# Kernel optimization log

Measured on AMD Instinct MI355X. Metric: run time of the kernel, lower is better.

Reference implementation:

```python
import jax, jax.numpy as jnp
import numpy as np

R, K, CF, HF, WF = 64, 81, 256, 256, 256  # ROIs, classes(incl bg), FPN channels, P2 size
IMG = 1024.0
SCALE = 0.25          # P2 feature stride 4
STEPS = 4             # subdivision steps: 7 -> 112
NPTS = 28 * 28        # subdivision_num_points
FC = 256


def _grid_sample(img, coords):
    """torch.grid_sample(bilinear, align_corners=False, zeros padding).
    img: [N,C,H,W]; coords: [N,P,2] (x,y) in [0,1]. Returns [N,C,P]."""
    N, C, H, W = img.shape
    x = coords[..., 0] * W - 0.5
    y = coords[..., 1] * H - 0.5
    x0 = jnp.floor(x); y0 = jnp.floor(y)
    fx = x - x0; fy = y - y0

    def g(ix, iy, w):
        valid = (ix >= 0) & (ix < W) & (iy >= 0) & (iy < H)
        ixc = jnp.clip(ix, 0, W - 1).astype(jnp.int32)
        iyc = jnp.clip(iy, 0, H - 1).astype(jnp.int32)
        v = jax.vmap(lambda im, yy, xx: im[:, yy, xx])(img, iyc, ixc)  # [N,C,P]
        return v * (w * valid)[:, None, :]

    return (g(x0, y0, (1 - fx) * (1 - fy)) + g(x0 + 1, y0, fx * (1 - fy))
            + g(x0, y0 + 1, (1 - fx) * fy) + g(x0 + 1, y0 + 1, fx * fy))


def _point_head(fine, coarse, W1, b1, W2, b2, W3, b3, Wp, bp):
    # StandardPointHead: 1x1-conv fc layers, coarse logits re-concatenated each layer
    x = jnp.concatenate([fine, coarse], axis=1)  # [R, CF+K, P]
    for Wl, bl in ((W1, b1), (W2, b2), (W3, b3)):
        x = jax.nn.relu(jnp.einsum('oc,rcp->rop', Wl, x) + bl[None, :, None])
        x = jnp.concatenate([x, coarse], axis=1)
    return jnp.einsum('oc,rcp->rop', Wp, x) + bp[None, :, None]  # [R,K,P]


def setup_inputs() -> dict:
    key = jax.random.key(0)
    ks = jax.random.split(key, 12)
    feat = jax.random.normal(ks[0], (1, CF, HF, WF), dtype=jnp.float32)
    u = jax.random.uniform(ks[1], (R, 4), dtype=jnp.float32)
    x0 = u[:, 0] * (IMG - 256.0); y0 = u[:, 1] * (IMG - 256.0)
    w = 32.0 + u[:, 2] * 224.0;   h = 32.0 + u[:, 3] * 224.0
    det_bboxes = jnp.stack([x0, y0, x0 + w, y0 + h], axis=1)
    det_labels = jax.random.randint(ks[2], (R,), 0, 80, dtype=jnp.int32)
    coarse_logits = jax.random.normal(ks[3], (R, K, 7, 7), dtype=jnp.float32)
    cin = CF + K  # = FC + K = 337 for all layers here
    s = 0.02
    return {
        'feat': feat, 'det_bboxes': det_bboxes, 'det_labels': det_labels,
        'coarse_logits': coarse_logits,
        'W1': jax.random.normal(ks[4], (FC, cin), jnp.float32) * s,
        'b1': jnp.zeros((FC,), jnp.float32),
        'W2': jax.random.normal(ks[5], (FC, FC + K), jnp.float32) * s,
        'b2': jnp.zeros((FC,), jnp.float32),
        'W3': jax.random.normal(ks[6], (FC, FC + K), jnp.float32) * s,
        'b3': jnp.zeros((FC,), jnp.float32),
        'Wp': jax.random.normal(ks[7], (K, FC + K), jnp.float32) * s,
        'bp': jnp.zeros((K,), jnp.float32),
    }


def reference(feat, det_bboxes, det_labels, coarse_logits,
              W1, b1, W2, b2, W3, b3, Wp, bp):
    ml = coarse_logits
    bx0, by0 = det_bboxes[:, 0], det_bboxes[:, 1]
    bw = det_bboxes[:, 2] - det_bboxes[:, 0]
    bh = det_bboxes[:, 3] - det_bboxes[:, 1]
    for step in range(STEPS):
        _, _, H, W = ml.shape
        H, W = 2 * H, 2 * W
        # bilinear x2, align_corners=False (half-pixel centers)
        ml = jax.image.resize(ml, (R, K, H, W), method='linear')
        if NPTS >= 4 * H * W and step < STEPS - 1:
            continue
        # uncertainty = -|logit of gt class| (det_labels+1 skips background ch 0)
        gt = ml[jnp.arange(R), det_labels + 1]              # [R,H,W]
        unc = -jnp.abs(gt).reshape(R, H * W)
        _, idx = jax.lax.top_k(unc, NPTS)                   # [R,NPTS]
        px = ((idx % W).astype(ml.dtype) + 0.5) / W
        py = ((idx // W).astype(ml.dtype) + 0.5) / H
        coords = jnp.stack([px, py], axis=-1)               # [R,NPTS,2] in ROI [0,1]
        # project ROI coords to image, then to P2 normalized coords
        cx = bx0[:, None] + coords[..., 0] * bw[:, None]
        cy = by0[:, None] + coords[..., 1] * bh[:, None]
        fcoords = jnp.stack([cx * SCALE / WF, cy * SCALE / HF], axis=-1)
        fine = _grid_sample(feat, fcoords.reshape(1, R * NPTS, 2))  # [1,CF,R*NPTS]
        fine = fine[0].reshape(CF, R, NPTS).transpose(1, 0, 2)      # [R,CF,NPTS]
        coarse = _grid_sample(coarse_logits, coords)                # [R,K,NPTS]
        pl = _point_head(fine, coarse, W1, b1, W2, b2, W3, b3, Wp, bp)
        ml = jax.vmap(lambda m, i, p: m.at[:, i].set(p))(
            ml.reshape(R, K, H * W), idx, pl).reshape(R, K, H, W)
    return ml
```

## Files before the change

kernel.cpp:

```cpp
#include <hip/hip_runtime.h>
#include <hip/hip_bf16.h>
#include <cstdint>
#include <cstddef>

#define R_ 64
#define K_ 81
#define NPTS_ 784

typedef __attribute__((ext_vector_type(8))) short short8;
typedef __attribute__((ext_vector_type(4))) float f32x4;

#define GLDS16(G, L)                                                           \
  __builtin_amdgcn_global_load_lds(                                            \
      (__attribute__((address_space(1))) void*)(void*)(G),                     \
      (__attribute__((address_space(3))) void*)(L), 16, 0, 0)

__global__ __launch_bounds__(256) void transpose_feat_kernel(const float* __restrict__ in,
                                                             float* __restrict__ out) {
  __shared__ float tile[32][33];
  int y = blockIdx.z;
  int x0 = blockIdx.x * 32, c0 = blockIdx.y * 32;
  int tx = threadIdx.x, ty = threadIdx.y;
#pragma unroll
  for (int j = 0; j < 32; j += 8)
    tile[ty + j][tx] = in[(size_t)(c0 + ty + j) * 65536 + (size_t)y * 256 + x0 + tx];
  __syncthreads();
#pragma unroll
  for (int j = 0; j < 32; j += 8)
    out[((size_t)y * 256 + (x0 + ty + j)) * 256 + c0 + tx] = tile[tx][ty + j];
}

__global__ void prep_all_kernel(const float* __restrict__ W1, const float* __restrict__ W2,
                                const float* __restrict__ W3, const float* __restrict__ Wp,
                                const float* __restrict__ b1, const float* __restrict__ b2,
                                const float* __restrict__ b3, const float* __restrict__ bp,
                                const float* __restrict__ coarse_in,
                                __hip_bfloat16* __restrict__ Wpk, float* __restrict__ bias_all,
                                float* __restrict__ coarseT) {
  int t = blockIdx.x * 256 + threadIdx.x;
  if (t < 90112) {
    int lane = t & 63;
    int t2 = t >> 6;
    int hl = t2 & 1;
    t2 >>= 1;
    int jg = t2 & 15;
    t2 >>= 4;
    int kt = t2 % 11;
    int L = t2 / 11;
    int o = jg * 16 + (lane & 15);
    int kbase = kt * 32 + (lane >> 4) * 8;
    const float* Wsrc = (L == 0) ? W1 : (L == 1) ? W2 : (L == 2) ? W3 : Wp;
    int Omax = (L == 3) ? 81 : 256;
    __hip_bfloat16 outv[8];
#pragma unroll
    for (int e = 0; e < 8; ++e) {
      int k = kbase + e;
      float v = (o < Omax && k < 337) ? Wsrc[o * 337 + k] : 0.f;
      __hip_bfloat16 h = __float2bfloat16(v);
      outv[e] = hl ? __float2bfloat16(v - __bfloat162float(h)) : h;
    }
    *(short8*)(Wpk + (size_t)t * 8) = *(const short8*)outv;
  } else if (t < 90112 + 1024) {
    int k = t - 90112;
    float v = 0.f;
    if (k < 256) v = b1[k];
    else if (k < 512) v = b2[k - 256];
    else if (k < 768) v = b3[k - 512];
    else if (k < 768 + 81) v = bp[k - 768];
    bias_all[k] = v;
  } else {
    int t2 = t - 91136;
    if (t2 < R_ * 49 * K_) {
      int k = t2 % K_;
      int t3 = t2 / K_;
      int pos = t3 % 49;
      int r = t3 / 49;
      coarseT[t2] = coarse_in[((size_t)r * K_ + k) * 49 + pos];
    }
  }
}

__device__ __forceinline__ void quad_upsample(const float* __restrict__ p, int Hin, int Win,
                                              int iy, int ix, float& oTE, float& oTO,
                                              float& oBE, float& oBO) {
  int rT = (iy == 0) ? 0 : iy - 1;
  int rB = (iy == Hin - 1) ? iy : iy + 1;
  int cL = (ix == 0) ? 0 : ix - 1;
  int cR = (ix == Win - 1) ? ix : ix + 1;
  float wyT1 = (iy == 0) ? 0.f : 0.75f;
  float wyB1 = (iy == Hin - 1) ? 0.f : 0.25f;
  float wxE1 = (ix == 0) ? 0.f : 0.75f;
  float wxO1 = (ix == Win - 1) ? 0.f : 0.25f;
  float wyT0 = 1.f - wyT1, wyB0 = 1.f - wyB1;
  float wxE0 = 1.f - wxE1, wxO0 = 1.f - wxO1;
  const float* rowA = p + (size_t)rT * Win;
  const float* rowM = p + (size_t)iy * Win;
  const float* rowC = p + (size_t)rB * Win;
  float al = rowA[cL], am = rowA[ix], ar = rowA[cR];
  float mL = rowM[cL], mm = rowM[ix], mr = rowM[cR];
  float cl = rowC[cL], cm = rowC[ix], cr = rowC[cR];
  float aE = wxE0 * al + wxE1 * am;
  float aO = wxO0 * am + wxO1 * ar;
  float mE = wxE0 * mL + wxE1 * mm;
  float mO = wxO0 * mm + wxO1 * mr;
  float cE = wxE0 * cl + wxE1 * cm;
  float cO = wxO0 * cm + wxO1 * cr;
  oTE = wyT0 * aE + wyT1 * mE;
  oTO = wyT0 * aO + wyT1 * mO;
  oBE = wyB0 * mE + wyB1 * cE;
  oBO = wyB0 * mO + wyB1 * cO;
}

__global__ __launch_bounds__(128) void upsample2x_kernel(const float* __restrict__ in,
                                                         float* __restrict__ out,
                                                         int Hin, int Win) {
  int b = blockIdx.z;
  int iy = blockIdx.y * 2 + threadIdx.y;
  int ix = blockIdx.x * 64 + threadIdx.x;
  if (ix >= Win || iy >= Hin) return;
  const float* p = in + (size_t)b * Hin * Win;
  float oTE, oTO, oBE, oBO;
  quad_upsample(p, Hin, Win, iy, ix, oTE, oTO, oBE, oBO);
  int Wout = 2 * Win;
  float* ob = out + ((size_t)b * (2 * Hin) + 2 * iy) * Wout + 2 * ix;
  *(float2*)ob = make_float2(oTE, oTO);
  *(float2*)(ob + Wout) = make_float2(oBE, oBO);
}

__global__ __launch_bounds__(128) void upsample2x_gt_kernel(const float* __restrict__ ml56,
                                                            const int* __restrict__ labels,
                                                            float* __restrict__ gtbuf) {
  int r = blockIdx.z;
  int iy = blockIdx.y * 2 + threadIdx.y;
  int ix = blockIdx.x * 64 + threadIdx.x;
  if (ix >= 56 || iy >= 56) return;
  const float* p = ml56 + ((size_t)r * K_ + (labels[r] + 1)) * 3136;
  float oTE, oTO, oBE, oBO;
  quad_upsample(p, 56, 56, iy, ix, oTE, oTO, oBE, oBO);
  float* ob = gtbuf + ((size_t)r * 112 + 2 * iy) * 112 + 2 * ix;
  *(float2*)ob = make_float2(oTE, oTO);
  *(float2*)(ob + 112) = make_float2(oBE, oBO);
}

__global__ __launch_bounds__(128) void upsample2x_sel_kernel(const float* __restrict__ ml56,
                                                             const unsigned short* __restrict__ map,
                                                             const float* __restrict__ PL,
                                                             float* __restrict__ out) {
  int b = blockIdx.z;
  int r = b / K_;
  int k = b - r * K_;
  int iy = blockIdx.y * 2 + threadIdx.y;
  int ix = blockIdx.x * 64 + threadIdx.x;
  if (ix >= 56 || iy >= 56) return;
  const float* p = ml56 + (size_t)b * 3136;
  float oTE, oTO, oBE, oBO;
  quad_upsample(p, 56, 56, iy, ix, oTE, oTO, oBE, oBO);
  int oy = 2 * iy, ox = 2 * ix;
  const unsigned short* mr = map + (size_t)r * 12544;
  unsigned short r0 = mr[oy * 112 + ox], r1 = mr[oy * 112 + ox + 1];
  unsigned short r2 = mr[(oy + 1) * 112 + ox], r3 = mr[(oy + 1) * 112 + ox + 1];
  if (r0 != 0xFFFFu) oTE = PL[((size_t)r * NPTS_ + r0) * 128 + k];
  if (r1 != 0xFFFFu) oTO = PL[((size_t)r * NPTS_ + r1) * 128 + k];
  if (r2 != 0xFFFFu) oBE = PL[((size_t)r * NPTS_ + r2) * 128 + k];
  if (r3 != 0xFFFFu) oBO = PL[((size_t)r * NPTS_ + r3) * 128 + k];
  float* ob = out + ((size_t)b * 112 + oy) * 112 + ox;
  *(float2*)ob = make_float2(oTE, oTO);
  *(float2*)(ob + 112) = make_float2(oBE, oBO);
}

__global__ void mapinit_kernel(unsigned short* __restrict__ map) {
  int t = blockIdx.x * 256 + threadIdx.x;
  if (t < R_ * 12544) map[t] = 0xFFFFu;
}
__global__ void mapbuild_kernel(const int* __restrict__ sel, unsigned short* __restrict__ map) {
  int t = blockIdx.x * 256 + threadIdx.x;
  if (t < R_ * NPTS_) {
    int r = t / NPTS_;
    map[(size_t)r * 12544 + sel[t]] = (unsigned short)(t % NPTS_);
  }
}

__global__ __launch_bounds__(1024) void topk_kernel(const float* __restrict__ ml,
                                                    const int* __restrict__ labels,
                                                    const float* __restrict__ gtdirect,
                                                    int N, int* __restrict__ sel) {
  int r = blockIdx.x;
  const float* gt = gtdirect ? (gtdirect + (size_t)r * N)
                             : (ml + ((size_t)r * K_ + (labels[r] + 1)) * N);
  __shared__ unsigned int hist[256];
  __shared__ unsigned int sh_prefix, sh_remaining, sh_countless;
  __shared__ unsigned int wtot_less[16], wtot_eq[16];
  const int tid = threadIdx.x;
  const int lane = tid & 63;
  const int wv = tid >> 6;

  unsigned int prefix = 0;
  unsigned int remaining = NPTS_;
  unsigned int count_less = 0;
  for (int pass = 0; pass < 4; ++pass) {
    int shift = 24 - 8 * pass;
    if (tid < 256) hist[tid] = 0;
    __syncthreads();
    for (int i = tid; i < N; i += 1024) {
      unsigned int v = __float_as_uint(fabsf(gt[i]));
      bool match = (pass == 0) || ((v >> (shift + 8)) == prefix);
      unsigned int dg = (v >> shift) & 255u;
      if (pass == 0) {
        bool active = match;
        while (true) {
          unsigned long long act = __ballot(active);
          if (!act) break;
          int leader = (int)(__ffsll((long long)act) - 1);
          unsigned int ld = __shfl(dg, leader);
          bool same = active && (dg == ld);
          unsigned long long sm = __ballot(same);
          if (lane == leader) atomicAdd(&hist[ld], (unsigned int)__popcll(sm));
          active = active && !same;
        }
      } else if (match) {
        atomicAdd(&hist[dg], 1u);
      }
    }
    __syncthreads();
    if (tid < 64) {
      unsigned int s0 = hist[4 * lane + 0], s1 = hist[4 * lane + 1];
      unsigned int s2 = hist[4 * lane + 2], s3 = hist[4 * lane + 3];
      unsigned int ls = s0 + s1 + s2 + s3;
      unsigned int inc = ls;
#pragma unroll
      for (int d = 1; d < 64; d <<= 1) {
        unsigned int tv = __shfl_up(inc, d);
        if (lane >= d) inc += tv;
      }
      unsigned int exc = inc - ls;
      bool cross = (exc < remaining) && (exc + ls >= remaining);
      if (cross) {
        unsigned int before = exc;
        int d = 4 * lane;
        if (before + s0 < remaining) {
          before += s0; d++;
          if (before + s1 < remaining) {
            before += s1; d++;
            if (before + s2 < remaining) { before += s2; d++; }
          }
        }
        sh_prefix = (prefix << 8) | (unsigned int)d;
        sh_remaining = remaining - before;
        sh_countless = count_less + before;
      }
    }
    __syncthreads();
    prefix = sh_prefix;
    remaining = sh_remaining;
    count_less = sh_countless;
    __syncthreads();
  }
  unsigned int vstar = prefix;
  unsigned int need_eq = NPTS_ - count_less;

  unsigned int base_less = 0, base_eq = 0;
  int* selr = sel + (size_t)r * NPTS_;
  for (int base = 0; base < N; base += 1024) {
    int i = base + tid;
    bool less = false, eq = false;
    if (i < N) {
      unsigned int v = __float_as_uint(fabsf(gt[i]));
      less = v < vstar;
      eq = v == vstar;
    }
    unsigned long long ml_ = __ballot(less);
    unsigned long long me_ = __ballot(eq);
    unsigned long long lanemask = (lane == 0) ? 0ull : ((~0ull) >> (64 - lane));
    unsigned int pl = __popcll(ml_ & lanemask);
    unsigned int pe = __popcll(me_ & lanemask);
    if (lane == 0) {
      wtot_less[wv] = (unsigned int)__popcll(ml_);
      wtot_eq[wv] = (unsigned int)__popcll(me_);
    }
    __syncthreads();
    unsigned int off_l = 0, off_e = 0, tot_l = 0, tot_e = 0;
#pragma unroll
    for (int w2 = 0; w2 < 16; ++w2) {
      unsigned int tl = wtot_less[w2], te = wtot_eq[w2];
      if (w2 < wv) { off_l += tl; off_e += te; }
      tot_l += tl;
      tot_e += te;
    }
    if (less) selr[base_less + off_l + pl] = i;
    if (eq) {
      unsigned int er = base_eq + off_e + pe;
      if (er < need_eq) selr[count_less + er] = i;
    }
    base_less += tot_l;
    base_eq += tot_e;
    __syncthreads();
  }
}

__global__ __launch_bounds__(256) void sample_kernel(const int* __restrict__ sel,
                                                     const float* __restrict__ bboxes,
                                                     const float* __restrict__ featT,
                                                     const float* __restrict__ coarseT,
                                                     __hip_bfloat16* __restrict__ Xh,
                                                     __hip_bfloat16* __restrict__ Xl,
                                                     __hip_bfloat16* __restrict__ Cth,
                                                     __hip_bfloat16* __restrict__ Ctl,
                                                     int Wlev, int Hlev) {
  int rp = blockIdx.x;
  int r = rp / NPTS_;
  int idx = sel ? sel[rp] : (rp % NPTS_);
  int tid = threadIdx.x;

  float px = ((float)(idx % Wlev) + 0.5f) / (float)Wlev;
  float py = ((float)(idx / Wlev) + 0.5f) / (float)Hlev;
  float bx0 = bboxes[r * 4 + 0], by0 = bboxes[r * 4 + 1];
  float bw = __fsub_rn(bboxes[r * 4 + 2], bx0);
  float bh = __fsub_rn(bboxes[r * 4 + 3], by0);
  float cx = __fadd_rn(bx0, __fmul_rn(px, bw));
  float cy = __fadd_rn(by0, __fmul_rn(py, bh));

  {
    float gx = __fsub_rn(__fmul_rn(cx, 0.25f), 0.5f);
    float gy = __fsub_rn(__fmul_rn(cy, 0.25f), 0.5f);
    float fxf = floorf(gx), fyf = floorf(gy);
    float fx = __fsub_rn(gx, fxf), fy = __fsub_rn(gy, fyf);
    int x0 = (int)fxf, y0 = (int)fyf;
    float ofx = __fsub_rn(1.f, fx), ofy = __fsub_rn(1.f, fy);
    float w00 = __fmul_rn(ofx, ofy);
    float w10 = __fmul_rn(fx, ofy);
    float w01 = __fmul_rn(ofx, fy);
    float w11 = __fmul_rn(fx, fy);
    bool vx0 = (x0 >= 0) && (x0 < 256), vx1 = (x0 + 1 >= 0) && (x0 + 1 < 256);
    bool vy0 = (y0 >= 0) && (y0 < 256), vy1 = (y0 + 1 >= 0) && (y0 + 1 < 256);
    float W00 = (vx0 && vy0) ? w00 : 0.f;
    float W10 = (vx1 && vy0) ? w10 : 0.f;
    float W01 = (vx0 && vy1) ? w01 : 0.f;
    float W11 = (vx1 && vy1) ? w11 : 0.f;
    int x0c = min(max(x0, 0), 255), x1c = min(max(x0 + 1, 0), 255);
    int y0c = min(max(y0, 0), 255), y1c = min(max(y0 + 1, 0), 255);
    const float* p00 = featT + ((size_t)(y0c * 256 + x0c)) * 256;
    const float* p10 = featT + ((size_t)(y0c * 256 + x1c)) * 256;
    const float* p01 = featT + ((size_t)(y1c * 256 + x0c)) * 256;
    const float* p11 = featT + ((size_t)(y1c * 256 + x1c)) * 256;
    float acc = __fmul_rn(p00[tid], W00);
    acc = __fadd_rn(acc, __fmul_rn(p10[tid], W10));
    acc = __fadd_rn(acc, __fmul_rn(p01[tid], W01));
    acc = __fadd_rn(acc, __fmul_rn(p11[tid], W11));
    __hip_bfloat16 h = __float2bfloat16(acc);
    Xh[(size_t)rp * 256 + tid] = h;
    Xl[(size_t)rp * 256 + tid] = __float2bfloat16(acc - __bfloat162float(h));
  }

  if (tid < 96) {
    float acc = 0.f;
    if (tid < K_) {
      float gx = __fsub_rn(__fmul_rn(px, 7.f), 0.5f);
      float gy = __fsub_rn(__fmul_rn(py, 7.f), 0.5f);
      float fxf = floorf(gx), fyf = floorf(gy);
      float fx = __fsub_rn(gx, fxf), fy = __fsub_rn(gy, fyf);
      int x0 = (int)fxf, y0 = (int)fyf;
      float ofx = __fsub_rn(1.f, fx), ofy = __fsub_rn(1.f, fy);
      float w00 = __fmul_rn(ofx, ofy);
      float w10 = __fmul_rn(fx, ofy);
      float w01 = __fmul_rn(ofx, fy);
      float w11 = __fmul_rn(fx, fy);
      bool vx0 = (x0 >= 0) && (x0 < 7), vx1 = (x0 + 1 >= 0) && (x0 + 1 < 7);
      bool vy0 = (y0 >= 0) && (y0 < 7), vy1 = (y0 + 1 >= 0) && (y0 + 1 < 7);
      float W00 = (vx0 && vy0) ? w00 : 0.f;
      float W10 = (vx1 && vy0) ? w10 : 0.f;
      float W01 = (vx0 && vy1) ? w01 : 0.f;
      float W11 = (vx1 && vy1) ? w11 : 0.f;
      int x0c = min(max(x0, 0), 6), x1c = min(max(x0 + 1, 0), 6);
      int y0c = min(max(y0, 0), 6), y1c = min(max(y0 + 1, 0), 6);
      const float* cb = coarseT + (size_t)r * 49 * K_;
      acc = __fmul_rn(cb[(size_t)(y0c * 7 + x0c) * K_ + tid], W00);
      acc = __fadd_rn(acc, __fmul_rn(cb[(size_t)(y0c * 7 + x1c) * K_ + tid], W10));
      acc = __fadd_rn(acc, __fmul_rn(cb[(size_t)(y1c * 7 + x0c) * K_ + tid], W01));
      acc = __fadd_rn(acc, __fmul_rn(cb[(size_t)(y1c * 7 + x1c) * K_ + tid], W11));
    }
    __hip_bfloat16 h = __float2bfloat16(acc);
    Cth[(size_t)rp * 96 + tid] = h;
    Ctl[(size_t)rp * 96 + tid] = __float2bfloat16(acc - __bfloat162float(h));
  }
}

template <int TERMS>
__global__ __launch_bounds__(256, 2) void fused_head_kernel(
    const __hip_bfloat16* __restrict__ Ah, const __hip_bfloat16* __restrict__ Al,
    const __hip_bfloat16* __restrict__ Th, const __hip_bfloat16* __restrict__ Tl,
    const __hip_bfloat16* __restrict__ Wpk,
    const float* __restrict__ bias_all, float* __restrict__ PL) {
  constexpr int XPLANE = 11 * 4096;
  constexpr int XLO = 8 * 4096;
  __shared__ char lds[(TERMS == 3) ? XPLANE + XLO : XPLANE];
  char* Xh = lds;
  char* Xl = lds + XPLANE;

  const int tid = threadIdx.x;
  const int lane = tid & 63;
  const int w = tid >> 6;
  const int g = lane >> 4;
  const int lane15 = lane & 15;
  const int m0 = blockIdx.x * 64;

  {
    const int srow = tid >> 2;
    const int sp = tid & 3;
    const int sx = sp ^ ((srow >> 1) & 3);
#pragma unroll
    for (int kt = 0; kt < 8; ++kt) {
      size_t off = (((size_t)(m0 + srow)) * 256 + (size_t)kt * 32 + (size_t)sx * 8) * 2;
      GLDS16((const char*)Ah + off, Xh + kt * 4096 + w * 1024);
      if constexpr (TERMS == 3) GLDS16((const char*)Al + off, Xl + kt * 4096 + w * 1024);
    }
#pragma unroll
    for (int kt = 8; kt < 11; ++kt) {
      size_t off = (((size_t)(m0 + srow)) * 96 + (size_t)(kt - 8) * 32 + (size_t)sx * 8) * 2;
      GLDS16((const char*)Th + off, Xh + kt * 4096 + w * 1024);
    }
  }
  asm volatile("s_waitcnt vmcnt(0)" ::: "memory");
  __syncthreads();

  int offA[4];
#pragma unroll
  for (int i = 0; i < 4; ++i) {
    int rowA = i * 16 + lane15;
    offA[i] = rowA * 64 + ((g ^ ((rowA >> 1) & 3)) << 4);
  }

#pragma unroll 1
  for (int L = 0; L < 4; ++L) {
    if (L == 3 && w >= 2) break;
    const __hip_bfloat16* WL = Wpk + (size_t)L * (11 * 16 * 2 * 512);

    f32x4 acc[4][4];
#pragma unroll
    for (int i = 0; i < 4; ++i)
#pragma unroll
      for (int j = 0; j < 4; ++j) acc[i][j] = (f32x4){0.f, 0.f, 0.f, 0.f};

    short8 a_h[4], a_l[4], b_h[2][4], b_l[2][4], tl_buf[2][4];

    auto loadB = [&](int buf, int kt) {
#pragma unroll
      for (int j = 0; j < 4; ++j) {
        const __hip_bfloat16* bp =
            WL + (((size_t)kt * 16 + (w * 4 + j)) * 2) * 512 + (size_t)lane * 8;
        b_h[buf][j] = *(const short8*)bp;
        if constexpr (TERMS == 3) b_l[buf][j] = *(const short8*)(bp + 512);
      }
    };
    auto loadTl = [&](int buf, int kt) {
#pragma unroll
      for (int i = 0; i < 4; ++i)
        tl_buf[buf][i] = *(const short8*)((const char*)Tl +
            (((size_t)(m0 + i * 16 + lane15)) * 96 + (size_t)(kt - 8) * 32 +
             (size_t)g * 8) * 2);
    };

    loadB(0, 0);

#pragma unroll
    for (int kt = 0; kt < 11; ++kt) {
      const int cb = kt & 1;
      if (kt < 10) {
        loadB(cb ^ 1, kt + 1);
        if constexpr (TERMS == 3) {
          if (kt + 1 >= 8) loadTl((kt + 1) & 1, kt + 1);
        }
      }
      __builtin_amdgcn_sched_barrier(0);
#pragma unroll
      for (int i = 0; i < 4; ++i) {
        a_h[i] = *(const short8*)(Xh + kt * 4096 + offA[i]);
        if constexpr (TERMS == 3) {
          if (kt < 8)
            a_l[i] = *(const short8*)(Xl + kt * 4096 + offA[i]);
          else
            a_l[i] = tl_buf[kt & 1][i];
        }
      }
      __builtin_amdgcn_s_setprio(1);
#pragma unroll
      for (int i = 0; i < 4; ++i)
#pragma unroll
        for (int j = 0; j < 4; ++j) {
          acc[i][j] = __builtin_amdgcn_mfma_f32_16x16x32_bf16(a_h[i], b_h[cb][j], acc[i][j], 0, 0, 0);
          if constexpr (TERMS == 3) {
            acc[i][j] = __builtin_amdgcn_mfma_f32_16x16x32_bf16(a_h[i], b_l[cb][j], acc[i][j], 0, 0, 0);
            acc[i][j] = __builtin_amdgcn_mfma_f32_16x16x32_bf16(a_l[i], b_h[cb][j], acc[i][j], 0, 0, 0);
          }
        }
      __builtin_amdgcn_s_setprio(0);
      __builtin_amdgcn_sched_barrier(0);
    }

    if (L < 3) {
      __syncthreads();
#pragma unroll
      for (int j = 0; j < 4; ++j) {
        int o = w * 64 + j * 16 + lane15;
        float bv = bias_all[L * 256 + o];
        int kch = o >> 5;
        int s0 = (o >> 3) & 3;
        int e = o & 7;
#pragma unroll
        for (int i = 0; i < 4; ++i) {
          int mb = i * 16 + g * 4;
#pragma unroll
          for (int r = 0; r < 4; ++r) {
            int m = mb + r;
            float v = fmaxf(acc[i][j][r] + bv, 0.f);
            __hip_bfloat16 h = __float2bfloat16(v);
            int boff = kch * 4096 + m * 64 + ((s0 ^ ((m >> 1) & 3)) << 4) + e * 2;
            *(__hip_bfloat16*)(Xh + boff) = h;
            if constexpr (TERMS == 3)
              *(__hip_bfloat16*)(Xl + boff) = __float2bfloat16(v - __bfloat162float(h));
          }
        }
      }
      __syncthreads();
    } else {
#pragma unroll
      for (int j = 0; j < 4; ++j) {
        int o = w * 64 + j * 16 + lane15;
        float bv = bias_all[768 + o];
#pragma unroll
        for (int i = 0; i < 4; ++i) {
          int mb = i * 16 + g * 4;
#pragma unroll
          for (int r = 0; r < 4; ++r)
            PL[(size_t)(m0 + mb + r) * 128 + o] = acc[i][j][r] + bv;
        }
      }
    }
  }
}

__global__ void scatter_kernel(const float* __restrict__ PL, const int* __restrict__ sel,
                               float* __restrict__ ml, int Nlev) {
  int t = blockIdx.x * 256 + threadIdx.x;
  if (t >= R_ * NPTS_ * K_) return;
  int k = t % K_;
  int rp = t / K_;
  int i = sel ? sel[rp] : (rp % NPTS_);
  int r = rp / NPTS_;
  ml[((size_t)r * K_ + k) * Nlev + i] = PL[(size_t)rp * 128 + k];
}

extern "C" void kernel_launch(void* const* d_in, const int* in_sizes, int n_in,
                              void* d_out, int out_size, void* d_ws, size_t ws_size,
                              hipStream_t stream) {
  (void)in_sizes; (void)n_in; (void)out_size; (void)ws_size;
  const float* feat = (const float*)d_in[0];
  const float* bboxes = (const float*)d_in[1];
  const int* labels = (const int*)d_in[2];
  const float* coarse = (const float*)d_in[3];
  const float* W1 = (const float*)d_in[4];
  const float* b1 = (const float*)d_in[5];
  const float* W2 = (const float*)d_in[6];
  const float* b2 = (const float*)d_in[7];
  const float* W3 = (const float*)d_in[8];
  const float* b3 = (const float*)d_in[9];
  const float* Wp = (const float*)d_in[10];
  const float* bp = (const float*)d_in[11];
  float* out = (float*)d_out;

  char* p = (char*)d_ws;
  auto alloc = [&](size_t bytes) { char* r = p; p += (bytes + 255) & ~(size_t)255; return r; };
  float* featT = (float*)alloc(16777216ull * 4);
  float* coarseT = (float*)alloc(254016ull * 4);
  float* ml28 = (float*)alloc(4064256ull * 4);
  float* ml56 = (float*)alloc(16257024ull * 4);
  float* PL = (float*)alloc(6422528ull * 4);
  int* sel = (int*)alloc(50176ull * 4);
  float* gtbuf = (float*)alloc(802816ull * 4);
  unsigned short* map = (unsigned short*)alloc(802816ull * 2);
  __hip_bfloat16* Xa_h = (__hip_bfloat16*)alloc(12845056ull * 2);
  __hip_bfloat16* Xa_l = (__hip_bfloat16*)alloc(12845056ull * 2);
  __hip_bfloat16* Ct_h = (__hip_bfloat16*)alloc(4816896ull * 2);
  __hip_bfloat16* Ct_l = (__hip_bfloat16*)alloc(4816896ull * 2);
  __hip_bfloat16* Wpk = (__hip_bfloat16*)alloc(720896ull * 2);
  float* bias_all = (float*)alloc(1024ull * 4);

  const int N = R_ * NPTS_;
  const int B = R_ * K_;

  transpose_feat_kernel<<<dim3(8, 8, 256), dim3(32, 8), 0, stream>>>(feat, featT);
  prep_all_kernel<<<1349, 256, 0, stream>>>(W1, W2, W3, Wp, b1, b2, b3, bp, coarse, Wpk, bias_all, coarseT);
  mapinit_kernel<<<3136, 256, 0, stream>>>(map);

  sample_kernel<<<N, 256, 0, stream>>>(nullptr, bboxes, featT, coarseT, Xa_h, Xa_l, Ct_h, Ct_l, 28, 28);
  fused_head_kernel<3><<<784, 256, 0, stream>>>(Xa_h, Xa_l, Ct_h, Ct_l, Wpk, bias_all, PL);
  scatter_kernel<<<15876, 256, 0, stream>>>(PL, nullptr, ml28, 784);

  upsample2x_kernel<<<dim3(1, 14, B), dim3(64, 2), 0, stream>>>(ml28, ml56, 28, 28);
  topk_kernel<<<R_, 1024, 0, stream>>>(ml56, labels, nullptr, 3136, sel);
  sample_kernel<<<N, 256, 0, stream>>>(sel, bboxes, featT, coarseT, Xa_h, Xa_l, Ct_h, Ct_l, 56, 56);
  fused_head_kernel<3><<<784, 256, 0, stream>>>(Xa_h, Xa_l, Ct_h, Ct_l, Wpk, bias_all, PL);
  scatter_kernel<<<15876, 256, 0, stream>>>(PL, sel, ml56, 3136);

  upsample2x_gt_kernel<<<dim3(1, 28, R_), dim3(64, 2), 0, stream>>>(ml56, labels, gtbuf);
  topk_kernel<<<R_, 1024, 0, stream>>>(nullptr, labels, gtbuf, 12544, sel);
  sample_kernel<<<N, 256, 0, stream>>>(sel, bboxes, featT, coarseT, Xa_h, Xa_l, Ct_h, Ct_l, 112, 112);
  fused_head_kernel<1><<<784, 256, 0, stream>>>(Xa_h, nullptr, Ct_h, nullptr, Wpk, bias_all, PL);
  mapbuild_kernel<<<196, 256, 0, stream>>>(sel, map);
  upsample2x_sel_kernel<<<dim3(1, 28, B), dim3(64, 2), 0, stream>>>(ml56, map, PL, out);
}
```

Measured before the change: 763.9 us.

## Widen 3-term head tile to 128 rows, fuse gt upsample into topk, merge map init

The three-term bf16-split point-head kernel now handles 128 rows per block (392 blocks, one block per CU, about 152KB of LDS), so each weight fragment loaded is reused across twice as many rows. The 112x112 ground-truth upsample is computed directly into shared memory inside a new topk kernel, removing the gtbuf global round trip and one launch. The map initialisation is folded into the prep kernel. The trade-off is lower occupancy and more register pressure (8x4 accumulator tiles) in the head kernel, which may limit latency hiding.

```diff
diff --git a/kernel.cpp b/kernel.cpp
--- a/kernel.cpp
+++ b/kernel.cpp
@@ -36,7 +36,7 @@
                                 const float* __restrict__ b3, const float* __restrict__ bp,
                                 const float* __restrict__ coarse_in,
                                 __hip_bfloat16* __restrict__ Wpk, float* __restrict__ bias_all,
-                                float* __restrict__ coarseT) {
+                                float* __restrict__ coarseT, unsigned short* __restrict__ map) {
   int t = blockIdx.x * 256 + threadIdx.x;
   if (t < 90112) {
     int lane = t & 63;
@@ -68,15 +68,16 @@
     else if (k < 768) v = b3[k - 512];
     else if (k < 768 + 81) v = bp[k - 768];
     bias_all[k] = v;
+  } else if (t < 91136 + 254016) {
+    int t2 = t - 91136;
+    int k = t2 % K_;
+    int t3 = t2 / K_;
+    int pos = t3 % 49;
+    int r = t3 / 49;
+    coarseT[t2] = coarse_in[((size_t)r * K_ + k) * 49 + pos];
   } else {
-    int t2 = t - 91136;
-    if (t2 < R_ * 49 * K_) {
-      int k = t2 % K_;
-      int t3 = t2 / K_;
-      int pos = t3 % 49;
-      int r = t3 / 49;
-      coarseT[t2] = coarse_in[((size_t)r * K_ + k) * 49 + pos];
-    }
+    int t2 = t - 345152;
+    if (t2 < R_ * 12544) map[t2] = 0xFFFFu;
   }
 }
 
@@ -127,21 +128,6 @@
   *(float2*)(ob + Wout) = make_float2(oBE, oBO);
 }
 
-__global__ __launch_bounds__(128) void upsample2x_gt_kernel(const float* __restrict__ ml56,
-                                                            const int* __restrict__ labels,
-                                                            float* __restrict__ gtbuf) {
-  int r = blockIdx.z;
-  int iy = blockIdx.y * 2 + threadIdx.y;
-  int ix = blockIdx.x * 64 + threadIdx.x;
-  if (ix >= 56 || iy >= 56) return;
-  const float* p = ml56 + ((size_t)r * K_ + (labels[r] + 1)) * 3136;
-  float oTE, oTO, oBE, oBO;
-  quad_upsample(p, 56, 56, iy, ix, oTE, oTO, oBE, oBO);
-  float* ob = gtbuf + ((size_t)r * 112 + 2 * iy) * 112 + 2 * ix;
-  *(float2*)ob = make_float2(oTE, oTO);
-  *(float2*)(ob + 112) = make_float2(oBE, oBO);
-}
-
 __global__ __launch_bounds__(128) void upsample2x_sel_kernel(const float* __restrict__ ml56,
                                                              const unsigned short* __restrict__ map,
                                                              const float* __restrict__ PL,
@@ -168,10 +154,6 @@
   *(float2*)(ob + 112) = make_float2(oBE, oBO);
 }
 
-__global__ void mapinit_kernel(unsigned short* __restrict__ map) {
-  int t = blockIdx.x * 256 + threadIdx.x;
-  if (t < R_ * 12544) map[t] = 0xFFFFu;
-}
 __global__ void mapbuild_kernel(const int* __restrict__ sel, unsigned short* __restrict__ map) {
   int t = blockIdx.x * 256 + threadIdx.x;
   if (t < R_ * NPTS_) {
@@ -180,19 +162,17 @@
   }
 }
 
-__global__ __launch_bounds__(1024) void topk_kernel(const float* __restrict__ ml,
-                                                    const int* __restrict__ labels,
-                                                    const float* __restrict__ gtdirect,
-                                                    int N, int* __restrict__ sel) {
-  int r = blockIdx.x;
-  const float* gt = gtdirect ? (gtdirect + (size_t)r * N)
-                             : (ml + ((size_t)r * K_ + (labels[r] + 1)) * N);
+template <bool LDSRC>
+__device__ void topk_core(const float* __restrict__ gt, const float* __restrict__ gtl,
+                          int N, int* __restrict__ selr) {
   __shared__ unsigned int hist[256];
   __shared__ unsigned int sh_prefix, sh_remaining, sh_countless;
   __shared__ unsigned int wtot_less[16], wtot_eq[16];
   const int tid = threadIdx.x;
   const int lane = tid & 63;
   const int wv = tid >> 6;
+
+  auto rd = [&](int i) -> float { return LDSRC ? gtl[i] : gt[i]; };
 
   unsigned int prefix = 0;
   unsigned int remaining = NPTS_;
@@ -202,7 +182,7 @@
     if (tid < 256) hist[tid] = 0;
     __syncthreads();
     for (int i = tid; i < N; i += 1024) {
-      unsigned int v = __float_as_uint(fabsf(gt[i]));
+      unsigned int v = __float_as_uint(fabsf(rd(i)));
       bool match = (pass == 0) || ((v >> (shift + 8)) == prefix);
       unsigned int dg = (v >> shift) & 255u;
       if (pass == 0) {
@@ -259,12 +239,11 @@
   unsigned int need_eq = NPTS_ - count_less;
 
   unsigned int base_less = 0, base_eq = 0;
-  int* selr = sel + (size_t)r * NPTS_;
   for (int base = 0; base < N; base += 1024) {
     int i = base + tid;
     bool less = false, eq = false;
     if (i < N) {
-      unsigned int v = __float_as_uint(fabsf(gt[i]));
+      unsigned int v = __float_as_uint(fabsf(rd(i)));
       less = v < vstar;
       eq = v == vstar;
     }
@@ -295,6 +274,35 @@
     base_eq += tot_e;
     __syncthreads();
   }
+}
+
+__global__ __launch_bounds__(1024) void topk_kernel(const float* __restrict__ ml,
+                                                    const int* __restrict__ labels,
+                                                    int N, int* __restrict__ sel) {
+  int r = blockIdx.x;
+  const float* gt = ml + ((size_t)r * K_ + (labels[r] + 1)) * N;
+  topk_core<false>(gt, nullptr, N, sel + (size_t)r * NPTS_);
+}
+
+__global__ __launch_bounds__(1024) void topk_gt_kernel(const float* __restrict__ ml56,
+                                                       const int* __restrict__ labels,
+                                                       int* __restrict__ sel) {
+  __shared__ float gtls[12544];
+  int r = blockIdx.x;
+  const float* p = ml56 + ((size_t)r * K_ + (labels[r] + 1)) * 3136;
+  int tid = threadIdx.x;
+  for (int t = tid; t < 3136; t += 1024) {
+    int iy = t / 56, ix = t % 56;
+    float oTE, oTO, oBE, oBO;
+    quad_upsample(p, 56, 56, iy, ix, oTE, oTO, oBE, oBO);
+    int oy = 2 * iy, ox = 2 * ix;
+    gtls[oy * 112 + ox] = oTE;
+    gtls[oy * 112 + ox + 1] = oTO;
+    gtls[(oy + 1) * 112 + ox] = oBE;
+    gtls[(oy + 1) * 112 + ox + 1] = oBO;
+  }
+  __syncthreads();
+  topk_core<true>(nullptr, gtls, 12544, sel + (size_t)r * NPTS_);
 }
 
 __global__ __launch_bounds__(256) void sample_kernel(const int* __restrict__ sel,
@@ -384,17 +392,160 @@
   }
 }
 
-template <int TERMS>
-__global__ __launch_bounds__(256, 2) void fused_head_kernel(
+__global__ __launch_bounds__(256, 1) void fused_head3_kernel(
     const __hip_bfloat16* __restrict__ Ah, const __hip_bfloat16* __restrict__ Al,
     const __hip_bfloat16* __restrict__ Th, const __hip_bfloat16* __restrict__ Tl,
     const __hip_bfloat16* __restrict__ Wpk,
     const float* __restrict__ bias_all, float* __restrict__ PL) {
-  constexpr int XPLANE = 11 * 4096;
-  constexpr int XLO = 8 * 4096;
-  __shared__ char lds[(TERMS == 3) ? XPLANE + XLO : XPLANE];
+  __shared__ char lds[155648];
   char* Xh = lds;
-  char* Xl = lds + XPLANE;
+  char* Xl = lds + 90112;
+
+  const int tid = threadIdx.x;
+  const int lane = tid & 63;
+  const int w = tid >> 6;
+  const int g = lane >> 4;
+  const int lane15 = lane & 15;
+  const int m0 = blockIdx.x * 128;
+
+  {
+    const int srow = tid >> 2;
+    const int sp = tid & 3;
+#pragma unroll
+    for (int c = 0; c < 2; ++c) {
+      const int row = c * 64 + srow;
+      const int sx = sp ^ ((row >> 1) & 3);
+#pragma unroll
+      for (int kt = 0; kt < 8; ++kt) {
+        size_t off = (((size_t)(m0 + row)) * 256 + (size_t)kt * 32 + (size_t)sx * 8) * 2;
+        GLDS16((const char*)Ah + off, Xh + kt * 8192 + c * 4096 + w * 1024);
+        GLDS16((const char*)Al + off, Xl + kt * 8192 + c * 4096 + w * 1024);
+      }
+#pragma unroll
+      for (int kt = 8; kt < 11; ++kt) {
+        size_t off = (((size_t)(m0 + row)) * 96 + (size_t)(kt - 8) * 32 + (size_t)sx * 8) * 2;
+        GLDS16((const char*)Th + off, Xh + kt * 8192 + c * 4096 + w * 1024);
+      }
+    }
+  }
+  asm volatile("s_waitcnt vmcnt(0)" ::: "memory");
+  __syncthreads();
+
+  int offA[8];
+#pragma unroll
+  for (int i = 0; i < 8; ++i) {
+    int rowA = i * 16 + lane15;
+    offA[i] = rowA * 64 + ((g ^ ((rowA >> 1) & 3)) << 4);
+  }
+
+#pragma unroll 1
+  for (int L = 0; L < 4; ++L) {
+    if (L == 3 && w >= 2) break;
+    const __hip_bfloat16* WL = Wpk + (size_t)L * (11 * 16 * 2 * 512);
+
+    f32x4 acc[8][4];
+#pragma unroll
+    for (int i = 0; i < 8; ++i)
+#pragma unroll
+      for (int j = 0; j < 4; ++j) acc[i][j] = (f32x4){0.f, 0.f, 0.f, 0.f};
+
+    short8 a_h[8], a_l[8], b_h[2][4], b_l[2][4], tl_buf[2][8];
+
+    auto loadB = [&](int buf, int kt) {
+#pragma unroll
+      for (int j = 0; j < 4; ++j) {
+        const __hip_bfloat16* bp =
+            WL + (((size_t)kt * 16 + (w * 4 + j)) * 2) * 512 + (size_t)lane * 8;
+        b_h[buf][j] = *(const short8*)bp;
+        b_l[buf][j] = *(const short8*)(bp + 512);
+      }
+    };
+    auto loadTl = [&](int buf, int kt) {
+#pragma unroll
+      for (int i = 0; i < 8; ++i)
+        tl_buf[buf][i] = *(const short8*)((const char*)Tl +
+            (((size_t)(m0 + i * 16 + lane15)) * 96 + (size_t)(kt - 8) * 32 +
+             (size_t)g * 8) * 2);
+    };
+
+    loadB(0, 0);
+
+#pragma unroll
+    for (int kt = 0; kt < 11; ++kt) {
+      const int cb = kt & 1;
+      if (kt < 10) {
+        loadB(cb ^ 1, kt + 1);
+        if (kt + 1 >= 8) loadTl((kt + 1) & 1, kt + 1);
+      }
+      __builtin_amdgcn_sched_barrier(0);
+#pragma unroll
+      for (int i = 0; i < 8; ++i) {
+        a_h[i] = *(const short8*)(Xh + kt * 8192 + offA[i]);
+        if (kt < 8)
+          a_l[i] = *(const short8*)(Xl + kt * 8192 + offA[i]);
+        else
+          a_l[i] = tl_buf[kt & 1][i];
+      }
+      __builtin_amdgcn_s_setprio(1);
+#pragma unroll
+      for (int i = 0; i < 8; ++i)
+#pragma unroll
+        for (int j = 0; j < 4; ++j) {
+          acc[i][j] = __builtin_amdgcn_mfma_f32_16x16x32_bf16(a_h[i], b_h[cb][j], acc[i][j], 0, 0, 0);
+          acc[i][j] = __builtin_amdgcn_mfma_f32_16x16x32_bf16(a_h[i], b_l[cb][j], acc[i][j], 0, 0, 0);
+          acc[i][j] = __builtin_amdgcn_mfma_f32_16x16x32_bf16(a_l[i], b_h[cb][j], acc[i][j], 0, 0, 0);
+        }
+      __builtin_amdgcn_s_setprio(0);
+      __builtin_amdgcn_sched_barrier(0);
+    }
+
+    if (L < 3) {
+      __syncthreads();
+#pragma unroll
+      for (int j = 0; j < 4; ++j) {
+        int o = w * 64 + j * 16 + lane15;
+        float bv = bias_all[L * 256 + o];
+        int kch = o >> 5;
+        int s0 = (o >> 3) & 3;
+        int e = o & 7;
+#pragma unroll
+        for (int i = 0; i < 8; ++i) {
+          int mb = i * 16 + g * 4;
+#pragma unroll
+          for (int r = 0; r < 4; ++r) {
+            int m = mb + r;
+            float v = fmaxf(acc[i][j][r] + bv, 0.f);
+            __hip_bfloat16 h = __float2bfloat16(v);
+            int boff = kch * 8192 + m * 64 + ((s0 ^ ((m >> 1) & 3)) << 4) + e * 2;
+            *(__hip_bfloat16*)(Xh + boff) = h;
+            *(__hip_bfloat16*)(Xl + boff) = __float2bfloat16(v - __bfloat162float(h));
+          }
+        }
+      }
+      __syncthreads();
+    } else {
+#pragma unroll
+      for (int j = 0; j < 4; ++j) {
+        int o = w * 64 + j * 16 + lane15;
+        float bv = bias_all[768 + o];
+#pragma unroll
+        for (int i = 0; i < 8; ++i) {
+          int mb = i * 16 + g * 4;
+#pragma unroll
+          for (int r = 0; r < 4; ++r)
+            PL[(size_t)(m0 + mb + r) * 128 + o] = acc[i][j][r] + bv;
+        }
+      }
+    }
+  }
+}
+
+__global__ __launch_bounds__(256, 2) void fused_head1_kernel(
+    const __hip_bfloat16* __restrict__ Ah, const __hip_bfloat16* __restrict__ Th,
+    const __hip_bfloat16* __restrict__ Wpk,
+    const float* __restrict__ bias_all, float* __restrict__ PL) {
+  __shared__ char lds[11 * 4096];
+  char* Xh = lds;
 
   const int tid = threadIdx.x;
   const int lane = tid & 63;
@@ -411,7 +562,6 @@
     for (int kt = 0; kt < 8; ++kt) {
       size_t off = (((size_t)(m0 + srow)) * 256 + (size_t)kt * 32 + (size_t)sx * 8) * 2;
       GLDS16((const char*)Ah + off, Xh + kt * 4096 + w * 1024);
-      if constexpr (TERMS == 3) GLDS16((const char*)Al + off, Xl + kt * 4096 + w * 1024);
     }
 #pragma unroll
     for (int kt = 8; kt < 11; ++kt) {
@@ -440,7 +590,7 @@
 #pragma unroll
       for (int j = 0; j < 4; ++j) acc[i][j] = (f32x4){0.f, 0.f, 0.f, 0.f};
 
-    short8 a_h[4], a_l[4], b_h[2][4], b_l[2][4], tl_buf[2][4];
+    short8 a_h[4], b_h[2][4];
 
     auto loadB = [&](int buf, int kt) {
 #pragma unroll
@@ -448,15 +598,7 @@
         const __hip_bfloat16* bp =
             WL + (((size_t)kt * 16 + (w * 4 + j)) * 2) * 512 + (size_t)lane * 8;
         b_h[buf][j] = *(const short8*)bp;
-        if constexpr (TERMS == 3) b_l[buf][j] = *(const short8*)(bp + 512);
-      }
-    };
-    auto loadTl = [&](int buf, int kt) {
-#pragma unroll
-      for (int i = 0; i < 4; ++i)
-        tl_buf[buf][i] = *(const short8*)((const char*)Tl +
-            (((size_t)(m0 + i * 16 + lane15)) * 96 + (size_t)(kt - 8) * 32 +
-             (size_t)g * 8) * 2);
+      }
     };
 
     loadB(0, 0);
@@ -464,34 +606,16 @@
 #pragma unroll
     for (int kt = 0; kt < 11; ++kt) {
       const int cb = kt & 1;
-      if (kt < 10) {
-        loadB(cb ^ 1, kt + 1);
-        if constexpr (TERMS == 3) {
-          if (kt + 1 >= 8) loadTl((kt + 1) & 1, kt + 1);
-        }
-      }
+      if (kt < 10) loadB(cb ^ 1, kt + 1);
       __builtin_amdgcn_sched_barrier(0);
 #pragma unroll
-      for (int i = 0; i < 4; ++i) {
-        a_h[i] = *(const short8*)(Xh + kt * 4096 + offA[i]);
-        if constexpr (TERMS == 3) {
-          if (kt < 8)
-            a_l[i] = *(const short8*)(Xl + kt * 4096 + offA[i]);
-          else
-            a_l[i] = tl_buf[kt & 1][i];
-        }
-      }
+      for (int i = 0; i < 4; ++i) a_h[i] = *(const short8*)(Xh + kt * 4096 + offA[i]);
       __builtin_amdgcn_s_setprio(1);
 #pragma unroll
       for (int i = 0; i < 4; ++i)
 #pragma unroll
-        for (int j = 0; j < 4; ++j) {
+        for (int j = 0; j < 4; ++j)
           acc[i][j] = __builtin_amdgcn_mfma_f32_16x16x32_bf16(a_h[i], b_h[cb][j], acc[i][j], 0, 0, 0);
-          if constexpr (TERMS == 3) {
-            acc[i][j] = __builtin_amdgcn_mfma_f32_16x16x32_bf16(a_h[i], b_l[cb][j], acc[i][j], 0, 0, 0);
-            acc[i][j] = __builtin_amdgcn_mfma_f32_16x16x32_bf16(a_l[i], b_h[cb][j], acc[i][j], 0, 0, 0);
-          }
-        }
       __builtin_amdgcn_s_setprio(0);
       __builtin_amdgcn_sched_barrier(0);
     }
@@ -512,11 +636,8 @@
           for (int r = 0; r < 4; ++r) {
             int m = mb + r;
             float v = fmaxf(acc[i][j][r] + bv, 0.f);
-            __hip_bfloat16 h = __float2bfloat16(v);
             int boff = kch * 4096 + m * 64 + ((s0 ^ ((m >> 1) & 3)) << 4) + e * 2;
-            *(__hip_bfloat16*)(Xh + boff) = h;
-            if constexpr (TERMS == 3)
-              *(__hip_bfloat16*)(Xl + boff) = __float2bfloat16(v - __bfloat162float(h));
+            *(__hip_bfloat16*)(Xh + boff) = __float2bfloat16(v);
           }
         }
       }
@@ -575,7 +696,6 @@
   float* ml56 = (float*)alloc(16257024ull * 4);
   float* PL = (float*)alloc(6422528ull * 4);
   int* sel = (int*)alloc(50176ull * 4);
-  float* gtbuf = (float*)alloc(802816ull * 4);
   unsigned short* map = (unsigned short*)alloc(802816ull * 2);
   __hip_bfloat16* Xa_h = (__hip_bfloat16*)alloc(12845056ull * 2);
   __hip_bfloat16* Xa_l = (__hip_bfloat16*)alloc(12845056ull * 2);
@@ -588,23 +708,21 @@
   const int B = R_ * K_;
 
   transpose_feat_kernel<<<dim3(8, 8, 256), dim3(32, 8), 0, stream>>>(feat, featT);
-  prep_all_kernel<<<1349, 256, 0, stream>>>(W1, W2, W3, Wp, b1, b2, b3, bp, coarse, Wpk, bias_all, coarseT);
-  mapinit_kernel<<<3136, 256, 0, stream>>>(map);
+  prep_all_kernel<<<4485, 256, 0, stream>>>(W1, W2, W3, Wp, b1, b2, b3, bp, coarse, Wpk, bias_all, coarseT, map);
 
   sample_kernel<<<N, 256, 0, stream>>>(nullptr, bboxes, featT, coarseT, Xa_h, Xa_l, Ct_h, Ct_l, 28, 28);
-  fused_head_kernel<3><<<784, 256, 0, stream>>>(Xa_h, Xa_l, Ct_h, Ct_l, Wpk, bias_all, PL);
+  fused_head3_kernel<<<392, 256, 0, stream>>>(Xa_h, Xa_l, Ct_h, Ct_l, Wpk, bias_all, PL);
   scatter_kernel<<<15876, 256, 0, stream>>>(PL, nullptr, ml28, 784);
 
   upsample2x_kernel<<<dim3(1, 14, B), dim3(64, 2), 0, stream>>>(ml28, ml56, 28, 28);
-  topk_kernel<<<R_, 1024, 0, stream>>>(ml56, labels, nullptr, 3136, sel);
+  topk_kernel<<<R_, 1024, 0, stream>>>(ml56, labels, 3136, sel);
   sample_kernel<<<N, 256, 0, stream>>>(sel, bboxes, featT, coarseT, Xa_h, Xa_l, Ct_h, Ct_l, 56, 56);
-  fused_head_kernel<3><<<784, 256, 0, stream>>>(Xa_h, Xa_l, Ct_h, Ct_l, Wpk, bias_all, PL);
+  fused_head3_kernel<<<392, 256, 0, stream>>>(Xa_h, Xa_l, Ct_h, Ct_l, Wpk, bias_all, PL);
   scatter_kernel<<<15876, 256, 0, stream>>>(PL, sel, ml56, 3136);
 
-  upsample2x_gt_kernel<<<dim3(1, 28, R_), dim3(64, 2), 0, stream>>>(ml56, labels, gtbuf);
-  topk_kernel<<<R_, 1024, 0, stream>>>(nullptr, labels, gtbuf, 12544, sel);
+  topk_gt_kernel<<<R_, 1024, 0, stream>>>(ml56, labels, sel);
   sample_kernel<<<N, 256, 0, stream>>>(sel, bboxes, featT, coarseT, Xa_h, Xa_l, Ct_h, Ct_l, 112, 112);
-  fused_head_kernel<1><<<784, 256, 0, stream>>>(Xa_h, nullptr, Ct_h, nullptr, Wpk, bias_all, PL);
+  fused_head1_kernel<<<784, 256, 0, stream>>>(Xa_h, Ct_h, Wpk, bias_all, PL);
   mapbuild_kernel<<<196, 256, 0, stream>>>(sel, map);
   upsample2x_sel_kernel<<<dim3(1, 28, B), dim3(64, 2), 0, stream>>>(ml56, map, PL, out);
 }
```

Result: slower. 792.0 us (+3.7%).

## Fuse scatter into upsample, upsample into top-k, and map init into prep

Applied to the files above, without the earlier changes.

At the first step, the upsample reads point-head logits straight from PL, which removes the scatter kernel and the ml28 buffer. At the last step, the gt-channel upsample is built inside the top-k kernel in shared memory, so the gtbuf round trip through global memory and one launch go away. Map initialization is folded into the prep kernel. The gains are fewer launches and less global traffic. The costs are strided PL reads (stride 128 floats) and about 49KB of LDS per top-k block, which may limit occupancy.

```diff
diff --git a/kernel.cpp b/kernel.cpp
--- a/kernel.cpp
+++ b/kernel.cpp
@@ -36,7 +36,7 @@
                                 const float* __restrict__ b3, const float* __restrict__ bp,
                                 const float* __restrict__ coarse_in,
                                 __hip_bfloat16* __restrict__ Wpk, float* __restrict__ bias_all,
-                                float* __restrict__ coarseT) {
+                                float* __restrict__ coarseT, unsigned short* __restrict__ map) {
   int t = blockIdx.x * 256 + threadIdx.x;
   if (t < 90112) {
     int lane = t & 63;
@@ -68,21 +68,22 @@
     else if (k < 768) v = b3[k - 512];
     else if (k < 768 + 81) v = bp[k - 768];
     bias_all[k] = v;
+  } else if (t < 91136 + 254016) {
+    int t2 = t - 91136;
+    int k = t2 % K_;
+    int t3 = t2 / K_;
+    int pos = t3 % 49;
+    int r = t3 / 49;
+    coarseT[t2] = coarse_in[((size_t)r * K_ + k) * 49 + pos];
   } else {
-    int t2 = t - 91136;
-    if (t2 < R_ * 49 * K_) {
-      int k = t2 % K_;
-      int t3 = t2 / K_;
-      int pos = t3 % 49;
-      int r = t3 / 49;
-      coarseT[t2] = coarse_in[((size_t)r * K_ + k) * 49 + pos];
-    }
-  }
-}
-
-__device__ __forceinline__ void quad_upsample(const float* __restrict__ p, int Hin, int Win,
-                                              int iy, int ix, float& oTE, float& oTO,
-                                              float& oBE, float& oBO) {
+    int t2 = t - 345152;
+    if (t2 < R_ * 12544) map[t2] = 0xFFFFu;
+  }
+}
+
+template <typename F>
+__device__ __forceinline__ void quad_upsample_g(F rd, int Hin, int Win, int iy, int ix,
+                                                float& oTE, float& oTO, float& oBE, float& oBO) {
   int rT = (iy == 0) ? 0 : iy - 1;
   int rB = (iy == Hin - 1) ? iy : iy + 1;
   int cL = (ix == 0) ? 0 : ix - 1;
@@ -93,12 +94,9 @@
   float wxO1 = (ix == Win - 1) ? 0.f : 0.25f;
   float wyT0 = 1.f - wyT1, wyB0 = 1.f - wyB1;
   float wxE0 = 1.f - wxE1, wxO0 = 1.f - wxO1;
-  const float* rowA = p + (size_t)rT * Win;
-  const float* rowM = p + (size_t)iy * Win;
-  const float* rowC = p + (size_t)rB * Win;
-  float al = rowA[cL], am = rowA[ix], ar = rowA[cR];
-  float mL = rowM[cL], mm = rowM[ix], mr = rowM[cR];
-  float cl = rowC[cL], cm = rowC[ix], cr = rowC[cR];
+  float al = rd(rT, cL), am = rd(rT, ix), ar = rd(rT, cR);
+  float mL = rd(iy, cL), mm = rd(iy, ix), mr = rd(iy, cR);
+  float cl = rd(rB, cL), cm = rd(rB, ix), cr = rd(rB, cR);
   float aE = wxE0 * al + wxE1 * am;
   float aO = wxO0 * am + wxO1 * ar;
   float mE = wxE0 * mL + wxE1 * mm;
@@ -111,35 +109,28 @@
   oBO = wyB0 * mO + wyB1 * cO;
 }
 
-__global__ __launch_bounds__(128) void upsample2x_kernel(const float* __restrict__ in,
-                                                         float* __restrict__ out,
-                                                         int Hin, int Win) {
+__device__ __forceinline__ void quad_upsample(const float* __restrict__ p, int Hin, int Win,
+                                              int iy, int ix, float& oTE, float& oTO,
+                                              float& oBE, float& oBO) {
+  quad_upsample_g([p, Win](int y, int x) { return p[(size_t)y * Win + x]; }, Hin, Win, iy, ix,
+                  oTE, oTO, oBE, oBO);
+}
+
+__global__ __launch_bounds__(128) void upsample2x_pl_kernel(const float* __restrict__ PL,
+                                                            float* __restrict__ out) {
   int b = blockIdx.z;
+  int r = b / K_;
+  int k = b - r * K_;
   int iy = blockIdx.y * 2 + threadIdx.y;
   int ix = blockIdx.x * 64 + threadIdx.x;
-  if (ix >= Win || iy >= Hin) return;
-  const float* p = in + (size_t)b * Hin * Win;
+  if (ix >= 28 || iy >= 28) return;
+  const float* base = PL + (size_t)r * NPTS_ * 128 + k;
   float oTE, oTO, oBE, oBO;
-  quad_upsample(p, Hin, Win, iy, ix, oTE, oTO, oBE, oBO);
-  int Wout = 2 * Win;
-  float* ob = out + ((size_t)b * (2 * Hin) + 2 * iy) * Wout + 2 * ix;
+  quad_upsample_g([base](int y, int x) { return base[(size_t)(y * 28 + x) * 128]; }, 28, 28,
+                  iy, ix, oTE, oTO, oBE, oBO);
+  float* ob = out + ((size_t)b * 56 + 2 * iy) * 56 + 2 * ix;
   *(float2*)ob = make_float2(oTE, oTO);
-  *(float2*)(ob + Wout) = make_float2(oBE, oBO);
-}
-
-__global__ __launch_bounds__(128) void upsample2x_gt_kernel(const float* __restrict__ ml56,
-                                                            const int* __restrict__ labels,
-                                                            float* __restrict__ gtbuf) {
-  int r = blockIdx.z;
-  int iy = blockIdx.y * 2 + threadIdx.y;
-  int ix = blockIdx.x * 64 + threadIdx.x;
-  if (ix >= 56 || iy >= 56) return;
-  const float* p = ml56 + ((size_t)r * K_ + (labels[r] + 1)) * 3136;
-  float oTE, oTO, oBE, oBO;
-  quad_upsample(p, 56, 56, iy, ix, oTE, oTO, oBE, oBO);
-  float* ob = gtbuf + ((size_t)r * 112 + 2 * iy) * 112 + 2 * ix;
-  *(float2*)ob = make_float2(oTE, oTO);
-  *(float2*)(ob + 112) = make_float2(oBE, oBO);
+  *(float2*)(ob + 56) = make_float2(oBE, oBO);
 }
 
 __global__ __launch_bounds__(128) void upsample2x_sel_kernel(const float* __restrict__ ml56,
@@ -168,10 +159,6 @@
   *(float2*)(ob + 112) = make_float2(oBE, oBO);
 }
 
-__global__ void mapinit_kernel(unsigned short* __restrict__ map) {
-  int t = blockIdx.x * 256 + threadIdx.x;
-  if (t < R_ * 12544) map[t] = 0xFFFFu;
-}
 __global__ void mapbuild_kernel(const int* __restrict__ sel, unsigned short* __restrict__ map) {
   int t = blockIdx.x * 256 + threadIdx.x;
   if (t < R_ * NPTS_) {
@@ -180,19 +167,17 @@
   }
 }
 
-__global__ __launch_bounds__(1024) void topk_kernel(const float* __restrict__ ml,
-                                                    const int* __restrict__ labels,
-                                                    const float* __restrict__ gtdirect,
-                                                    int N, int* __restrict__ sel) {
-  int r = blockIdx.x;
-  const float* gt = gtdirect ? (gtdirect + (size_t)r * N)
-                             : (ml + ((size_t)r * K_ + (labels[r] + 1)) * N);
+template <bool LDSRC>
+__device__ void topk_core(const float* __restrict__ gt, const float* __restrict__ gtl,
+                          int N, int* __restrict__ selr) {
   __shared__ unsigned int hist[256];
   __shared__ unsigned int sh_prefix, sh_remaining, sh_countless;
   __shared__ unsigned int wtot_less[16], wtot_eq[16];
   const int tid = threadIdx.x;
   const int lane = tid & 63;
   const int wv = tid >> 6;
+
+  auto rd = [&](int i) -> float { return LDSRC ? gtl[i] : gt[i]; };
 
   unsigned int prefix = 0;
   unsigned int remaining = NPTS_;
@@ -202,7 +187,7 @@
     if (tid < 256) hist[tid] = 0;
     __syncthreads();
     for (int i = tid; i < N; i += 1024) {
-      unsigned int v = __float_as_uint(fabsf(gt[i]));
+      unsigned int v = __float_as_uint(fabsf(rd(i)));
       bool match = (pass == 0) || ((v >> (shift + 8)) == prefix);
       unsigned int dg = (v >> shift) & 255u;
       if (pass == 0) {
@@ -259,12 +244,11 @@
   unsigned int need_eq = NPTS_ - count_less;
 
   unsigned int base_less = 0, base_eq = 0;
-  int* selr = sel + (size_t)r * NPTS_;
   for (int base = 0; base < N; base += 1024) {
     int i = base + tid;
     bool less = false, eq = false;
     if (i < N) {
-      unsigned int v = __float_as_uint(fabsf(gt[i]));
+      unsigned int v = __float_as_uint(fabsf(rd(i)));
       less = v < vstar;
       eq = v == vstar;
     }
@@ -295,6 +279,35 @@
     base_eq += tot_e;
     __syncthreads();
   }
+}
+
+__global__ __launch_bounds__(1024) void topk_kernel(const float* __restrict__ ml,
+                                                    const int* __restrict__ labels,
+                                                    int N, int* __restrict__ sel) {
+  int r = blockIdx.x;
+  const float* gt = ml + ((size_t)r * K_ + (labels[r] + 1)) * N;
+  topk_core<false>(gt, nullptr, N, sel + (size_t)r * NPTS_);
+}
+
+__global__ __launch_bounds__(1024) void topk_gt_kernel(const float* __restrict__ ml56,
+                                                       const int* __restrict__ labels,
+                                                       int* __restrict__ sel) {
+  __shared__ float gtls[12544];
+  int r = blockIdx.x;
+  const float* p = ml56 + ((size_t)r * K_ + (labels[r] + 1)) * 3136;
+  int tid = threadIdx.x;
+  for (int t = tid; t < 3136; t += 1024) {
+    int iy = t / 56, ix = t % 56;
+    float oTE, oTO, oBE, oBO;
+    quad_upsample(p, 56, 56, iy, ix, oTE, oTO, oBE, oBO);
+    int oy = 2 * iy, ox = 2 * ix;
+    gtls[oy * 112 + ox] = oTE;
+    gtls[oy * 112 + ox + 1] = oTO;
+    gtls[(oy + 1) * 112 + ox] = oBE;
+    gtls[(oy + 1) * 112 + ox + 1] = oBO;
+  }
+  __syncthreads();
+  topk_core<true>(nullptr, gtls, 12544, sel + (size_t)r * NPTS_);
 }
 
 __global__ __launch_bounds__(256) void sample_kernel(const int* __restrict__ sel,
@@ -571,11 +584,9 @@
   auto alloc = [&](size_t bytes) { char* r = p; p += (bytes + 255) & ~(size_t)255; return r; };
   float* featT = (float*)alloc(16777216ull * 4);
   float* coarseT = (float*)alloc(254016ull * 4);
-  float* ml28 = (float*)alloc(4064256ull * 4);
   float* ml56 = (float*)alloc(16257024ull * 4);
   float* PL = (float*)alloc(6422528ull * 4);
   int* sel = (int*)alloc(50176ull * 4);
-  float* gtbuf = (float*)alloc(802816ull * 4);
   unsigned short* map = (unsigned short*)alloc(802816ull * 2);
   __hip_bfloat16* Xa_h = (__hip_bfloat16*)alloc(12845056ull * 2);
   __hip_bfloat16* Xa_l = (__hip_bfloat16*)alloc(12845056ull * 2);
@@ -588,21 +599,18 @@
   const int B = R_ * K_;
 
   transpose_feat_kernel<<<dim3(8, 8, 256), dim3(32, 8), 0, stream>>>(feat, featT);
-  prep_all_kernel<<<1349, 256, 0, stream>>>(W1, W2, W3, Wp, b1, b2, b3, bp, coarse, Wpk, bias_all, coarseT);
-  mapinit_kernel<<<3136, 256, 0, stream>>>(map);
+  prep_all_kernel<<<4485, 256, 0, stream>>>(W1, W2, W3, Wp, b1, b2, b3, bp, coarse, Wpk, bias_all, coarseT, map);
 
   sample_kernel<<<N, 256, 0, stream>>>(nullptr, bboxes, featT, coarseT, Xa_h, Xa_l, Ct_h, Ct_l, 28, 28);
   fused_head_kernel<3><<<784, 256, 0, stream>>>(Xa_h, Xa_l, Ct_h, Ct_l, Wpk, bias_all, PL);
-  scatter_kernel<<<15876, 256, 0, stream>>>(PL, nullptr, ml28, 784);
-
-  upsample2x_kernel<<<dim3(1, 14, B), dim3(64, 2), 0, stream>>>(ml28, ml56, 28, 28);
-  topk_kernel<<<R_, 1024, 0, stream>>>(ml56, labels, nullptr, 3136, sel);
+
+  upsample2x_pl_kernel<<<dim3(1, 14, B), dim3(64, 2), 0, stream>>>(PL, ml56);
+  topk_kernel<<<R_, 1024, 0, stream>>>(ml56, labels, 3136, sel);
   sample_kernel<<<N, 256, 0, stream>>>(sel, bboxes, featT, coarseT, Xa_h, Xa_l, Ct_h, Ct_l, 56, 56);
   fused_head_kernel<3><<<784, 256, 0, stream>>>(Xa_h, Xa_l, Ct_h, Ct_l, Wpk, bias_all, PL);
   scatter_kernel<<<15876, 256, 0, stream>>>(PL, sel, ml56, 3136);
 
-  upsample2x_gt_kernel<<<dim3(1, 28, R_), dim3(64, 2), 0, stream>>>(ml56, labels, gtbuf);
-  topk_kernel<<<R_, 1024, 0, stream>>>(nullptr, labels, gtbuf, 12544, sel);
+  topk_gt_kernel<<<R_, 1024, 0, stream>>>(ml56, labels, sel);
   sample_kernel<<<N, 256, 0, stream>>>(sel, bboxes, featT, coarseT, Xa_h, Xa_l, Ct_h, Ct_l, 112, 112);
   fused_head_kernel<1><<<784, 256, 0, stream>>>(Xa_h, nullptr, Ct_h, nullptr, Wpk, bias_all, PL);
   mapbuild_kernel<<<196, 256, 0, stream>>>(sel, map);
```

Result: no change. 769.9 us (+0.8%).
